# Kernel optimization log

Measured on AMD Instinct MI355X. Metric: run time of the kernel, lower is better.

The kernel has to match this reference:

```python
import jax, jax.numpy as jnp
import numpy as np
from jax import lax

NUM_LAYERS, C, HIDDEN = 3, 64, 128
B, H, W = 16, 128, 128
DC = C // 4  # partial-conv channels (dim_conv = dim // 4)


def _conv2d(x, w, b=None, groups=1):
    # x: [B,C,H,W], w: [O, C//groups, kh, kw], SAME padding, stride 1
    y = lax.conv_general_dilated(x, w, (1, 1), 'SAME',
                                 dimension_numbers=('NCHW', 'OIHW', 'NCHW'),
                                 feature_group_count=groups)
    return y if b is None else y + b[None, :, None, None]


def _pw(x, w, b):
    # 1x1x1 Conv3d at T=1 == pointwise channel mix. w: [O, C], b: [O]
    return jnp.einsum('oc,bchw->bohw', w, x) + b[None, :, None, None]


def _gelu(x):
    return jax.nn.gelu(x, approximate=False)  # torch nn.GELU default (erf)


def setup_inputs() -> dict:
    key = jax.random.key(0)
    ks = jax.random.split(key, 18)
    s = 0.1
    return {
        'x': jax.random.normal(ks[0], (B, C, H, W), jnp.float32),
        'wz1': jax.random.normal(ks[1], (NUM_LAYERS, C, C), jnp.float32) * s,
        'bz1': jax.random.normal(ks[2], (NUM_LAYERS, C), jnp.float32) * s,
        'wz2': jax.random.normal(ks[3], (NUM_LAYERS, C, C), jnp.float32) * s,
        'bz2': jax.random.normal(ks[4], (NUM_LAYERS, C), jnp.float32) * s,
        'wf1': jax.random.normal(ks[5], (NUM_LAYERS, C, C), jnp.float32) * s,
        'bf1': jax.random.normal(ks[6], (NUM_LAYERS, C), jnp.float32) * s,
        'wf2': jax.random.normal(ks[7], (NUM_LAYERS, C, C), jnp.float32) * s,
        'bf2': jax.random.normal(ks[8], (NUM_LAYERS, C), jnp.float32) * s,
        # FRFN
        'pconv_w': jax.random.normal(ks[9], (NUM_LAYERS, DC, DC, 3, 3), jnp.float32) * s,
        'lin1_w': jax.random.normal(ks[10], (NUM_LAYERS, C, 2 * HIDDEN), jnp.float32) * s,
        'lin1_b': jax.random.normal(ks[11], (NUM_LAYERS, 2 * HIDDEN), jnp.float32) * s,
        'dw_w': jax.random.normal(ks[12], (NUM_LAYERS, HIDDEN, 1, 3, 3), jnp.float32) * s,
        'dw_b': jax.random.normal(ks[13], (NUM_LAYERS, HIDDEN), jnp.float32) * s,
        'lin2_w': jax.random.normal(ks[14], (NUM_LAYERS, HIDDEN, C), jnp.float32) * s,
        'lin2_b': jax.random.normal(ks[15], (NUM_LAYERS, C), jnp.float32) * s,
        # conv_out: in_dim -> out_dim=1, 3x3
        'out_w': jax.random.normal(ks[16], (1, C, 3, 3), jnp.float32) * s,
        'out_b': jax.random.normal(ks[17], (1,), jnp.float32) * s,
    }


def reference(x, wz1, bz1, wz2, bz2, wf1, bf1, wf2, bf2,
              pconv_w, lin1_w, lin1_b, dw_w, dw_b, lin2_w, lin2_b,
              out_w, out_b):
    x_init = x
    for l in range(NUM_LAYERS):
        # ---- MHRB: time dim is 1 (x.unsqueeze(2)), so flips over dim 2 are
        # identities and the recurrence is a single step h = (1 - F) * Z.
        Z = jnp.tanh(_pw(jnp.tanh(_pw(x, wz1[l], bz1[l])), wz2[l], bz2[l]))
        F = jax.nn.sigmoid(_pw(jnp.tanh(_pw(x, wf1[l], bf1[l])), wf2[l], bf2[l]))
        x = (1.0 - F) * Z
        # ---- FRFN (operates on b (h w) c; equivalently on NCHW channel dim)
        res = x
        x1 = _conv2d(x[:, :DC], pconv_w[l])            # partial 3x3 conv, no bias
        x = jnp.concatenate([x1, x[:, DC:]], axis=1)
        h = _gelu(jnp.einsum('bchw,ck->bkhw', x, lin1_w[l])
                  + lin1_b[l][None, :, None, None])    # linear1 + GELU
        h1, h2 = h[:, :HIDDEN], h[:, HIDDEN:]          # chunk(2, dim=-1)
        h1 = _gelu(_conv2d(h1, dw_w[l], dw_b[l], groups=HIDDEN))  # dwconv + GELU
        g = h1 * h2                                    # gating
        x = (jnp.einsum('bkhw,kc->bchw', g, lin2_w[l])
             + lin2_b[l][None, :, None, None]) + res   # linear2 + residual
    return _conv2d(x + x_init, out_w, out_b)           # conv_out
```

## Files before the change

### kernel.cpp

```cpp
#include <hip/hip_runtime.h>
#include <hip/hip_bf16.h>

#define CC 64
#define HIDN 128
#define DCC 16
#define HH 128
#define WW 128
#define HWS (HH*WW)
#define BB 16
#define NPIX (BB*HWS)

typedef __hip_bfloat16 bf16;
typedef __attribute__((ext_vector_type(8))) unsigned short ushort8;
typedef __attribute__((ext_vector_type(4))) unsigned short ushort4v;
typedef __attribute__((ext_vector_type(4))) float float4v;
typedef __attribute__((ext_vector_type(8))) short bf16x8;
typedef __attribute__((ext_vector_type(4))) float f32x4;

__device__ __forceinline__ float rcp_fast(float x){ return __builtin_amdgcn_rcpf(x); }
__device__ __forceinline__ float ftanh(float x){
    float e = __expf(2.f*x);
    return 1.f - 2.f*rcp_fast(e + 1.f);
}
__device__ __forceinline__ float fsig(float x){
    return rcp_fast(1.f + __expf(-x));
}
__device__ __forceinline__ float fgelu(float x){
    return x * fsig(x*(1.5957691216f + 0.07135481283f*x*x));
}
__device__ __forceinline__ float b2f(bf16 v){ return __bfloat162float(v); }
__device__ __forceinline__ float u2f(unsigned short u){
    unsigned v = ((unsigned)u) << 16; return __uint_as_float(v);
}
__device__ __forceinline__ unsigned short f2u(float f){
    bf16 h = __float2bfloat16(f);
    return *reinterpret_cast<unsigned short*>(&h);
}
__device__ __forceinline__ bf16x8 packf(float4v a, float4v b){
    bf16x8 r;
    r[0]=(short)f2u(a.x); r[1]=(short)f2u(a.y); r[2]=(short)f2u(a.z); r[3]=(short)f2u(a.w);
    r[4]=(short)f2u(b.x); r[5]=(short)f2u(b.y); r[6]=(short)f2u(b.z); r[7]=(short)f2u(b.w);
    return r;
}

template<int F32>
__global__ __launch_bounds__(256,2) void k_gate(
    const float* __restrict__ xf, const bf16* __restrict__ xb,
    const float* __restrict__ wz1, const float* __restrict__ bz1,
    const float* __restrict__ wz2, const float* __restrict__ bz2,
    const float* __restrict__ wf1, const float* __restrict__ bf1,
    const float* __restrict__ wf2, const float* __restrict__ bf2,
    bf16* __restrict__ vout)
{
    __shared__ __align__(16) unsigned short xs[512*64];
    const int t = threadIdx.x;
    const int lane = t & 63;
    const int wv = t >> 6;
    const int col = lane & 15;
    const int g = lane >> 4;
    const int blk = blockIdx.x;
    const int b = blk >> 5;
    const int sp0 = (blk & 31) << 9;

    {
        const int ch = t & 63;
        const int wg = t >> 6;
        const size_t base = ((size_t)b*CC + ch)*HWS + sp0;
        #pragma unroll
        for (int i=0;i<16;++i){
            int bufpx = (wg*16 + i) << 3;
            ushort8 val;
            if (F32){
                float4v a = *reinterpret_cast<const float4v*>(xf + base + bufpx);
                float4v c = *reinterpret_cast<const float4v*>(xf + base + bufpx + 4);
                val[0]=f2u(a.x); val[1]=f2u(a.y); val[2]=f2u(a.z); val[3]=f2u(a.w);
                val[4]=f2u(c.x); val[5]=f2u(c.y); val[6]=f2u(c.z); val[7]=f2u(c.w);
            } else {
                val = *reinterpret_cast<const ushort8*>(xb + base + bufpx);
            }
            #pragma unroll
            for (int j=0;j<8;++j){
                int px = bufpx + j;
                *(unsigned short*)((char*)xs + px*128 + ((ch*2) ^ ((px&7)<<4))) = val[j];
            }
        }
    }

    bf16x8 Az1[4][2], Af1[4][2], Az2[4][2], Af2[4][2];
    #pragma unroll
    for (int ot=0; ot<4; ++ot){
        #pragma unroll
        for (int kh=0; kh<2; ++kh){
            const float* p;
            p = wz1 + (ot*16+col)*64 + kh*32 + g*8;
            Az1[ot][kh] = packf(*(const float4v*)p, *(const float4v*)(p+4));
            p = wf1 + (ot*16+col)*64 + kh*32 + g*8;
            Af1[ot][kh] = packf(*(const float4v*)p, *(const float4v*)(p+4));
            p = wz2 + (ot*16+col)*64 + kh*32 + g*4;
            Az2[ot][kh] = packf(*(const float4v*)p, *(const float4v*)(p+16));
            p = wf2 + (ot*16+col)*64 + kh*32 + g*4;
            Af2[ot][kh] = packf(*(const float4v*)p, *(const float4v*)(p+16));
        }
    }
    __syncthreads();

    bf16* vb = vout + (size_t)b*CC*HWS;

    for (int it = wv; it < 32; it += 4){
        const int lpx = it*16 + col;
        const int px = sp0 + lpx;
        bf16x8 Bx[2];
        Bx[0] = *(const bf16x8*)((char*)xs + lpx*128 + ((g*16) ^ ((lpx&7)<<4)));
        Bx[1] = *(const bf16x8*)((char*)xs + lpx*128 + ((64 + g*16) ^ ((lpx&7)<<4)));
        f32x4 Dz[4], Df[4];
        #pragma unroll
        for (int ot=0; ot<4; ++ot){
            Dz[ot] = *(const f32x4*)(bz1 + ot*16 + g*4);
            Df[ot] = *(const f32x4*)(bf1 + ot*16 + g*4);
        }
        #pragma unroll
        for (int kh=0; kh<2; ++kh)
            #pragma unroll
            for (int ot=0; ot<4; ++ot){
                Dz[ot] = __builtin_amdgcn_mfma_f32_16x16x32_bf16(Az1[ot][kh], Bx[kh], Dz[ot], 0,0,0);
                Df[ot] = __builtin_amdgcn_mfma_f32_16x16x32_bf16(Af1[ot][kh], Bx[kh], Df[ot], 0,0,0);
            }
        #pragma unroll
        for (int ot=0; ot<4; ++ot)
            #pragma unroll
            for (int r=0; r<4; ++r){
                Dz[ot][r] = ftanh(Dz[ot][r]);
                Df[ot][r] = ftanh(Df[ot][r]);
            }
        bf16x8 Bz[2], Bf[2];
        #pragma unroll
        for (int kh=0; kh<2; ++kh)
            #pragma unroll
            for (int j=0; j<4; ++j){
                Bz[kh][j]   = (short)f2u(Dz[2*kh][j]);
                Bz[kh][4+j] = (short)f2u(Dz[2*kh+1][j]);
                Bf[kh][j]   = (short)f2u(Df[2*kh][j]);
                Bf[kh][4+j] = (short)f2u(Df[2*kh+1][j]);
            }
        f32x4 Ez[4], Ef[4];
        #pragma unroll
        for (int ot=0; ot<4; ++ot){
            Ez[ot] = *(const f32x4*)(bz2 + ot*16 + g*4);
            Ef[ot] = *(const f32x4*)(bf2 + ot*16 + g*4);
        }
        #pragma unroll
        for (int kh=0; kh<2; ++kh)
            #pragma unroll
            for (int ot=0; ot<4; ++ot){
                Ez[ot] = __builtin_amdgcn_mfma_f32_16x16x32_bf16(Az2[ot][kh], Bz[kh], Ez[ot], 0,0,0);
                Ef[ot] = __builtin_amdgcn_mfma_f32_16x16x32_bf16(Af2[ot][kh], Bf[kh], Ef[ot], 0,0,0);
            }
        #pragma unroll
        for (int ot=0; ot<4; ++ot)
            #pragma unroll
            for (int r=0; r<4; ++r){
                float Zv = ftanh(Ez[ot][r]);
                float Fv = fsig(Ef[ot][r]);
                *reinterpret_cast<unsigned short*>(vb + (size_t)(ot*16+g*4+r)*HWS + px)
                    = f2u((1.f - Fv)*Zv);
            }
    }
}

__global__ __launch_bounds__(256) void k_pl1(
    const bf16* __restrict__ v, const float* __restrict__ pw,
    const float* __restrict__ l1w, const float* __restrict__ l1b,
    bf16* __restrict__ x1out, bf16* __restrict__ h1out)
{
    __shared__ __align__(16) unsigned short xs[256*64];
    __shared__ __align__(16) unsigned short vh[16][4][128];
    __shared__ __align__(16) unsigned short tr[4][32*66];
    const int t = threadIdx.x;
    const int lane = t & 63;
    const int wv = t >> 6;
    const int col = lane & 15;
    const int g = lane >> 4;
    const int blk = blockIdx.x;
    const int b = blk >> 6;
    const int y0 = (blk & 63) << 1;
    const int sp0 = y0 * WW;

    {
        const int ch = t & 63;
        const int wg = t >> 6;
        if (ch < DCC){
            int gy = y0 - 1 + wg;
            unsigned short* dst = &vh[ch][wg][0];
            if (gy >= 0 && gy < HH){
                const bf16* src = v + ((size_t)b*CC + ch)*HWS + (size_t)gy*WW;
                #pragma unroll
                for (int i=0;i<16;++i)
                    *reinterpret_cast<ushort8*>(dst + i*8) =
                        *reinterpret_cast<const ushort8*>(src + i*8);
            } else {
                #pragma unroll
                for (int i=0;i<16;++i){
                    ushort8 z;
                    #pragma unroll
                    for (int j=0;j<8;++j) z[j]=0;
                    *reinterpret_cast<ushort8*>(dst + i*8) = z;
                }
            }
        } else {
            const bf16* src = v + ((size_t)b*CC + ch)*HWS + sp0;
            #pragma unroll
            for (int i=0;i<8;++i){
                int bufpx = wg*64 + i*8;
                ushort8 val = *reinterpret_cast<const ushort8*>(src + bufpx);
                #pragma unroll
                for (int j=0;j<8;++j){
                    int px = bufpx + j;
                    *(unsigned short*)((char*)xs + px*128 + ((ch*2) ^ ((px&7)<<4))) = val[j];
                }
            }
        }
    }
    __syncthreads();

    {
        const int oc = t >> 4;
        const int px0 = (t & 15) << 3;
        float acc[2][8];
        #pragma unroll
        for (int r=0;r<2;++r)
            #pragma unroll
            for (int i=0;i<8;++i) acc[r][i]=0.f;
        #pragma unroll 1
        for (int ic=0; ic<DCC; ++ic){
            float m[4][10];
            #pragma unroll
            for (int row=0;row<4;++row){
                const unsigned short* rp = &vh[ic][row][px0];
                ushort8 mv = *reinterpret_cast<const ushort8*>(rp);
                #pragma unroll
                for (int i=0;i<8;++i) m[row][i+1] = u2f(mv[i]);
                m[row][0] = (px0>0)    ? u2f(rp[-1]) : 0.f;
                m[row][9] = (px0+8<WW) ? u2f(rp[8])  : 0.f;
            }
            const float* wp = pw + (size_t)(oc*DCC+ic)*9;
            #pragma unroll
            for (int ky=0;ky<3;++ky){
                float w0 = wp[ky*3+0], w1 = wp[ky*3+1], w2 = wp[ky*3+2];
                #pragma unroll
                for (int r=0;r<2;++r)
                    #pragma unroll
                    for (int i=0;i<8;++i)
                        acc[r][i] = fmaf(w0, m[r+ky][i],
                                    fmaf(w1, m[r+ky][i+1],
                                    fmaf(w2, m[r+ky][i+2], acc[r][i])));
            }
        }
        #pragma unroll
        for (int r=0;r<2;++r){
            ushort8 ov;
            #pragma unroll
            for (int i=0;i<8;++i){
                unsigned short uu = f2u(acc[r][i]);
                ov[i] = uu;
                int px = r*128 + px0 + i;
                *(unsigned short*)((char*)xs + px*128 + ((oc*2) ^ ((px&7)<<4))) = uu;
            }
            *reinterpret_cast<ushort8*>(x1out + ((size_t)b*DCC + oc)*HWS
                                        + (size_t)(y0+r)*WW + px0) = ov;
        }
    }
    __syncthreads();

    unsigned short* trw = &tr[wv][0];
    const int lpx0 = wv*64;

    #pragma unroll 1
    for (int oc=0; oc<4; ++oc){
        bf16x8 A1[2][2];
        #pragma unroll
        for (int t2=0;t2<2;++t2)
            #pragma unroll
            for (int kh=0;kh<2;++kh){
                bf16x8 fa;
                #pragma unroll
                for (int j=0;j<8;++j){
                    int cin = kh*32 + g*8 + j;
                    fa[j] = (short)f2u(l1w[cin*256 + oc*32 + t2*16 + col]);
                }
                A1[t2][kh]=fa;
            }
        #pragma unroll
        for (int lt=0;lt<4;++lt){
            int px = lpx0 + lt*16 + col;
            bf16x8 B0 = *(const bf16x8*)((char*)xs + px*128 + ((g*16) ^ ((px&7)<<4)));
            bf16x8 B1 = *(const bf16x8*)((char*)xs + px*128 + ((64 + g*16) ^ ((px&7)<<4)));
            f32x4 D0 = *(const f32x4*)(l1b + oc*32 + g*4);
            f32x4 D1 = *(const f32x4*)(l1b + oc*32 + 16 + g*4);
            D0 = __builtin_amdgcn_mfma_f32_16x16x32_bf16(A1[0][0], B0, D0, 0,0,0);
            D0 = __builtin_amdgcn_mfma_f32_16x16x32_bf16(A1[0][1], B1, D0, 0,0,0);
            D1 = __builtin_amdgcn_mfma_f32_16x16x32_bf16(A1[1][0], B0, D1, 0,0,0);
            D1 = __builtin_amdgcn_mfma_f32_16x16x32_bf16(A1[1][1], B1, D1, 0,0,0);
            int lp = lt*16 + col;
            #pragma unroll
            for (int rr=0;rr<4;++rr){
                trw[(g*4+rr)*66 + lp]    = f2u(fgelu(D0[rr]));
                trw[(16+g*4+rr)*66 + lp] = f2u(fgelu(D1[rr]));
            }
        }
        {
            int ch2 = lane >> 1;
            int half = lane & 1;
            const unsigned short* srcp = trw + ch2*66 + half*32;
            bf16* dst = h1out + ((size_t)(b*HIDN + oc*32 + ch2))*HWS + sp0 + lpx0 + half*32;
            #pragma unroll
            for (int i=0;i<4;++i){
                ushort8 u8 = *reinterpret_cast<const ushort8*>(srcp + i*8);
                *reinterpret_cast<ushort8*>(dst + i*8) = u8;
            }
        }
    }
}

__global__ __launch_bounds__(256) void k_wprep(
    const float* __restrict__ l1w_all, const float* __restrict__ w2_all,
    bf16* __restrict__ frag_all)
{
    const int l = blockIdx.x;
    const float* l1w = l1w_all + (size_t)l*CC*256;
    const float* w2  = w2_all  + (size_t)l*HIDN*CC;
    unsigned short* buf1 = (unsigned short*)(frag_all + (size_t)l*16384);
    unsigned short* buf2 = buf1 + 8192;
    const int t = threadIdx.x;
    const int lane = t & 63;
    const int col = lane & 15;
    const int g = lane >> 4;
    #pragma unroll
    for (int c4=0;c4<4;++c4){
        int combo = (t>>6)*4 + c4;
        {
            int cc = combo >> 2, t2 = (combo>>1)&1, kh = combo&1;
            #pragma unroll
            for (int j=0;j<8;++j){
                int cin = kh*32 + g*8 + j;
                buf1[(combo*64 + lane)*8 + j] =
                    f2u(l1w[cin*256 + 128 + cc*32 + t2*16 + col]);
            }
        }
        {
            int cc = combo >> 2, ot = combo & 3;
            #pragma unroll
            for (int j=0;j<8;++j){
                int k = cc*32 + ((j>>2)<<4) + (g<<2) + (j&3);
                buf2[(combo*64 + lane)*8 + j] = f2u(w2[k*64 + ot*16 + col]);
            }
        }
    }
}

__global__ __launch_bounds__(256) void k_dwA(
    const bf16* __restrict__ x1, const bf16* __restrict__ v,
    const bf16* __restrict__ h1, const bf16* __restrict__ wfrag,
    const float* __restrict__ l1b,
    const float* __restrict__ dww, const float* __restrict__ dwb,
    const float* __restrict__ l2b,
    bf16* __restrict__ xout,
    const float* __restrict__ xinit,
    bf16* __restrict__ xsum)
{
    __shared__ __align__(16) unsigned short xs[128*64];
    __shared__ __align__(16) unsigned short ubuf[2*8320];
    const int t = threadIdx.x;
    const int lane = t & 63;
    const int wv = t >> 6;
    const int col = lane & 15;
    const int g = lane >> 4;
    const int blk0 = blockIdx.x;
    const int blk = (blk0 & 7)*256 + (blk0 >> 3);
    const int b = blk >> 7;
    const int y = blk & 127;

    const int cj  = (t>>3) & 31;
    const int pxo = (t & 7) << 4;

    const unsigned short* buf1 = (const unsigned short*)wfrag;
    const unsigned short* buf2 = buf1 + 8192;

    ushort8 pfa[3], pfb[3];
    unsigned short pfl[3], pfr[3];
    float pw9[9], pbj;
    auto LOADCHUNK = [&](int cc){
        int chg = cc*32 + cj;
        const bf16* h1p = h1 + ((size_t)(b*HIDN + chg))*HWS;
        #pragma unroll
        for (int ky=0; ky<3; ++ky){
            int gy = y + ky - 1;
            if (gy >= 0 && gy < HH){
                const bf16* rp = h1p + (size_t)gy*WW + pxo;
                pfa[ky] = *reinterpret_cast<const ushort8*>(rp);
                pfb[ky] = *reinterpret_cast<const ushort8*>(rp+8);
                pfl[ky] = (pxo>0)     ? *reinterpret_cast<const unsigned short*>(rp-1)  : 0;
                pfr[ky] = (pxo+16<WW) ? *reinterpret_cast<const unsigned short*>(rp+16) : 0;
            } else {
                #pragma unroll
                for (int i=0;i<8;++i){ pfa[ky][i]=0; pfb[ky][i]=0; }
                pfl[ky]=0; pfr[ky]=0;
            }
        }
        #pragma unroll
        for (int i=0;i<9;++i) pw9[i] = dww[chg*9+i];
        pbj = dwb[chg];
    };

    LOADCHUNK(0);

    {
        const int ch = t & 63;
        const int wg = t >> 6;
        const bf16* src = (ch < DCC) ? x1 + ((size_t)b*DCC + ch)*HWS
                                     : v  + ((size_t)b*CC  + ch)*HWS;
        #pragma unroll
        for (int i=0;i<2;++i){
            int bufpx = (wg*2 + i) << 3;
            ushort8 val = *reinterpret_cast<const ushort8*>(src + (size_t)y*WW + bufpx);
            #pragma unroll
            for (int j=0;j<8;++j){
                int px = bufpx + j;
                *(unsigned short*)((char*)xs + px*128 + ((ch*2) ^ ((px&7)<<4))) = val[j];
            }
        }
    }
    __syncthreads();

    f32x4 Dx[2][4];
    #pragma unroll
    for (int q=0;q<2;++q)
        #pragma unroll
        for (int ot=0;ot<4;++ot)
            Dx[q][ot] = *(const f32x4*)(l2b + ot*16 + g*4);

    #pragma unroll 1
    for (int cc=0; cc<4; ++cc){
        unsigned short* ub = ubuf + (cc&1)*8320;
        ushort8 o0v, o1v;
        {
            float acc[16];
            #pragma unroll
            for (int i=0;i<16;++i) acc[i]=0.f;
            #pragma unroll
            for (int ky=0; ky<3; ++ky){
                float m[16];
                #pragma unroll
                for (int i=0;i<8;++i){ m[i]=u2f(pfa[ky][i]); m[8+i]=u2f(pfb[ky][i]); }
                float lf = u2f(pfl[ky]);
                float rt = u2f(pfr[ky]);
                float w0=pw9[ky*3], w1=pw9[ky*3+1], wv2=pw9[ky*3+2];
                #pragma unroll
                for (int i=0;i<16;++i){
                    float l  = i ? m[i-1] : lf;
                    float r_ = (i==15) ? rt : m[i+1];
                    acc[i] = fmaf(w0,l, fmaf(w1,m[i], fmaf(wv2,r_,acc[i])));
                }
            }
            #pragma unroll
            for (int i=0;i<8;++i){
                o0v[i] = f2u(fgelu(acc[i]+pbj));
                o1v[i] = f2u(fgelu(acc[8+i]+pbj));
            }
        }
        if (cc < 3) LOADCHUNK(cc+1);
        *(ushort8*)(ub + cj*260 + pxo)     = o0v;
        *(ushort8*)(ub + cj*260 + pxo + 8) = o1v;
        __syncthreads();
        {
            bf16x8 A1g[2][2];
            #pragma unroll
            for (int t2=0;t2<2;++t2)
                #pragma unroll
                for (int kh=0;kh<2;++kh){
                    int combo = (cc*2+t2)*2+kh;
                    ushort8 u = *reinterpret_cast<const ushort8*>(buf1 + (combo*64 + lane)*8);
                    bf16x8 f;
                    #pragma unroll
                    for (int j=0;j<8;++j) f[j]=(short)u[j];
                    A1g[t2][kh]=f;
                }
            bf16x8 A2[4];
            #pragma unroll
            for (int ot=0;ot<4;++ot){
                int combo = cc*4+ot;
                ushort8 u = *reinterpret_cast<const ushort8*>(buf2 + (combo*64 + lane)*8);
                bf16x8 f;
                #pragma unroll
                for (int j=0;j<8;++j) f[j]=(short)u[j];
                A2[ot] = f;
            }
            #pragma unroll
            for (int q=0;q<2;++q){
                int px = (wv*2+q)*16 + col;
                bf16x8 B0 = *(const bf16x8*)((char*)xs + px*128 + ((g*16) ^ ((px&7)<<4)));
                bf16x8 B1 = *(const bf16x8*)((char*)xs + px*128 + ((64 + g*16) ^ ((px&7)<<4)));
                f32x4 D0 = *(const f32x4*)(l1b + 128 + cc*32 + g*4);
                f32x4 D1 = *(const f32x4*)(l1b + 128 + cc*32 + 16 + g*4);
                D0 = __builtin_amdgcn_mfma_f32_16x16x32_bf16(A1g[0][0], B0, D0, 0,0,0);
                D0 = __builtin_amdgcn_mfma_f32_16x16x32_bf16(A1g[0][1], B1, D0, 0,0,0);
                D1 = __builtin_amdgcn_mfma_f32_16x16x32_bf16(A1g[1][0], B0, D1, 0,0,0);
                D1 = __builtin_amdgcn_mfma_f32_16x16x32_bf16(A1g[1][1], B1, D1, 0,0,0);
                bf16x8 Bg;
                #pragma unroll
                for (int j=0;j<4;++j){
                    float u0 = u2f(ub[(g*4+j)*260 + px]);
                    float u1 = u2f(ub[(16+g*4+j)*260 + px]);
                    Bg[j]   = (short)f2u(u0 * fgelu(D0[j]));
                    Bg[4+j] = (short)f2u(u1 * fgelu(D1[j]));
                }
                #pragma unroll
                for (int ot=0;ot<4;++ot)
                    Dx[q][ot] = __builtin_amdgcn_mfma_f32_16x16x32_bf16(A2[ot], Bg, Dx[q][ot], 0,0,0);
            }
        }
    }
    __syncthreads();
    #pragma unroll
    for (int q=0;q<2;++q)
        #pragma unroll
        for (int ot=0;ot<4;++ot)
            #pragma unroll
            for (int rr=0;rr<4;++rr)
                ubuf[(ot*16 + g*4 + rr)*136 + (wv*2+q)*16 + col] = f2u(Dx[q][ot][rr]);
    __syncthreads();
    {
        int ch  = t >> 2;
        int pxb = (t & 3) * 32;
        size_t off = ((size_t)(b*CC + ch))*HWS + (size_t)y*WW + pxb;
        #pragma unroll
        for (int i=0;i<4;++i){
            ushort8 dv = *reinterpret_cast<const ushort8*>(ubuf + ch*136 + pxb + i*8);
            ushort8 vv = *reinterpret_cast<const ushort8*>(v + off + i*8);
            ushort8 ov;
            float rv[8];
            #pragma unroll
            for (int j=0;j<8;++j){
                rv[j] = u2f(dv[j]) + u2f(vv[j]);
                ov[j] = f2u(rv[j]);
            }
            *reinterpret_cast<ushort8*>(xout + off + i*8) = ov;
            if (xinit){
                float4v x0 = *reinterpret_cast<const float4v*>(xinit + off + i*8);
                float4v x1v = *reinterpret_cast<const float4v*>(xinit + off + i*8 + 4);
                ushort8 sv;
                sv[0]=f2u(rv[0]+x0.x); sv[1]=f2u(rv[1]+x0.y);
                sv[2]=f2u(rv[2]+x0.z); sv[3]=f2u(rv[3]+x0.w);
                sv[4]=f2u(rv[4]+x1v.x); sv[5]=f2u(rv[5]+x1v.y);
                sv[6]=f2u(rv[6]+x1v.z); sv[7]=f2u(rv[7]+x1v.w);
                *reinterpret_cast<ushort8*>(xsum + off + i*8) = sv;
            }
        }
    }
}

__global__ __launch_bounds__(256) void k_final(
    const bf16* __restrict__ s, const float* __restrict__ w,
    const float* __restrict__ bias, float* __restrict__ out)
{
    int gid = blockIdx.x*256 + threadIdx.x;
    int b = gid >> 11;
    int sp8 = (gid & 2047) << 3;
    int y = sp8 >> 7, x0 = sp8 & 127;
    const bf16* sb = s + (size_t)b*CC*HWS;
    float acc[8];
    #pragma unroll
    for (int i=0;i<8;++i) acc[i] = bias[0];

    #pragma unroll 1
    for (int c=0;c<CC;++c){
        const bf16* ip = sb + (size_t)c*HWS;
        const float* wp = w + (size_t)c*9;
        #pragma unroll
        for (int ky=0;ky<3;++ky){
            int yy = y + ky - 1;
            float xv[10];
            if (yy >= 0 && yy < HH){
                const bf16* rp = ip + yy*WW + x0;
                ushort8 mv = *reinterpret_cast<const ushort8*>(rp);
                #pragma unroll
                for (int i=0;i<8;++i) xv[i+1]=u2f(mv[i]);
                xv[0] = (x0>0)    ? b2f(rp[-1]) : 0.f;
                xv[9] = (x0+8<WW) ? b2f(rp[8])  : 0.f;
            } else {
                #pragma unroll
                for (int i=0;i<10;++i) xv[i] = 0.f;
            }
            float w0 = wp[ky*3+0], w1 = wp[ky*3+1], w2 = wp[ky*3+2];
            #pragma unroll
            for (int i=0;i<8;++i)
                acc[i] = fmaf(w0, xv[i],
                         fmaf(w1, xv[i+1],
                         fmaf(w2, xv[i+2], acc[i])));
        }
    }
    float4v o0, o1;
    o0.x=acc[0]; o0.y=acc[1]; o0.z=acc[2]; o0.w=acc[3];
    o1.x=acc[4]; o1.y=acc[5]; o1.z=acc[6]; o1.w=acc[7];
    float* op = out + (size_t)gid*8;
    *reinterpret_cast<float4v*>(op)     = o0;
    *reinterpret_cast<float4v*>(op + 4) = o1;
}

extern "C" void kernel_launch(void* const* d_in, const int* in_sizes, int n_in,
                              void* d_out, int out_size, void* d_ws, size_t ws_size,
                              hipStream_t stream)
{
    const float* x    = (const float*)d_in[0];
    const float* wz1  = (const float*)d_in[1];
    const float* bz1  = (const float*)d_in[2];
    const float* wz2  = (const float*)d_in[3];
    const float* bz2  = (const float*)d_in[4];
    const float* wf1  = (const float*)d_in[5];
    const float* bf1  = (const float*)d_in[6];
    const float* wf2  = (const float*)d_in[7];
    const float* bf2  = (const float*)d_in[8];
    const float* pw   = (const float*)d_in[9];
    const float* l1w  = (const float*)d_in[10];
    const float* l1b  = (const float*)d_in[11];
    const float* dww  = (const float*)d_in[12];
    const float* dwb  = (const float*)d_in[13];
    const float* l2w  = (const float*)d_in[14];
    const float* l2b  = (const float*)d_in[15];
    const float* ow   = (const float*)d_in[16];
    const float* obb  = (const float*)d_in[17];

    char* ws = (char*)d_ws;
    bf16* xc    = (bf16*)(ws);
    bf16* v     = (bf16*)(ws + 33554432);
    bf16* x1    = (bf16*)(ws + 67108864);
    bf16* xsumb = (bf16*)(ws + 75497472);
    bf16* h1buf = (bf16*)(ws + 109051904);
    bf16* wfrag = (bf16*)(ws + 176160768);

    k_wprep<<<3, 256, 0, stream>>>(l1w, l2w, wfrag);
    for (int l=0;l<3;++l){
        if (l == 0)
            k_gate<1><<<512, 256, 0, stream>>>(x, nullptr,
                wz1 + l*CC*CC, bz1 + l*CC, wz2 + l*CC*CC, bz2 + l*CC,
                wf1 + l*CC*CC, bf1 + l*CC, wf2 + l*CC*CC, bf2 + l*CC, v);
        else
            k_gate<0><<<512, 256, 0, stream>>>(nullptr, xc,
                wz1 + l*CC*CC, bz1 + l*CC, wz2 + l*CC*CC, bz2 + l*CC,
                wf1 + l*CC*CC, bf1 + l*CC, wf2 + l*CC*CC, bf2 + l*CC, v);
        k_pl1  <<<NPIX/256, 256, 0, stream>>>(v, pw + l*DCC*DCC*9,
                l1w + l*CC*256, l1b + l*256, x1, h1buf);
        k_dwA  <<<BB*HH, 256, 0, stream>>>(x1, v, h1buf, wfrag + (size_t)l*16384,
                l1b + l*256,
                dww + l*HIDN*9, dwb + l*HIDN,
                l2b + l*CC,
                xc, (l==2) ? x : nullptr, xsumb);
    }
    k_final<<<NPIX/(256*8), 256, 0, stream>>>(xsumb, ow, obb, (float*)d_out);
}
```

Before: 673.0 us.

## Process two image rows per block in fused dwconv/gating/linear2 kernel

Each k_dwA block now handles two adjacent output rows instead of one, halving the grid. The depthwise 3x3 loads four input rows per channel chunk instead of three per output row, which reuses the shared halo rows. Weight fragment loads are also amortized over twice as many pixels. The double-buffered ub is replaced by one buffer plus an extra barrier per chunk. This costs more registers (Dx doubles, extra prefetch rows) and larger LDS, so occupancy may drop.

```diff
diff --git a/kernel.cpp b/kernel.cpp
--- a/kernel.cpp
+++ b/kernel.cpp
@@ -367,17 +367,17 @@
     const float* __restrict__ xinit,
     bf16* __restrict__ xsum)
 {
-    __shared__ __align__(16) unsigned short xs[128*64];
-    __shared__ __align__(16) unsigned short ubuf[2*8320];
+    __shared__ __align__(16) unsigned short xs[256*64];
+    __shared__ __align__(16) unsigned short ub[64*264];
     const int t = threadIdx.x;
     const int lane = t & 63;
     const int wv = t >> 6;
     const int col = lane & 15;
     const int g = lane >> 4;
     const int blk0 = blockIdx.x;
-    const int blk = (blk0 & 7)*256 + (blk0 >> 3);
-    const int b = blk >> 7;
-    const int y = blk & 127;
+    const int blk = (blk0 & 7)*128 + (blk0 >> 3);
+    const int b = blk >> 6;
+    const int y0 = (blk & 63) << 1;
 
     const int cj  = (t>>3) & 31;
     const int pxo = (t & 7) << 4;
@@ -385,15 +385,15 @@
     const unsigned short* buf1 = (const unsigned short*)wfrag;
     const unsigned short* buf2 = buf1 + 8192;
 
-    ushort8 pfa[3], pfb[3];
-    unsigned short pfl[3], pfr[3];
+    ushort8 pfa[4], pfb[4];
+    unsigned short pfl[4], pfr[4];
     float pw9[9], pbj;
     auto LOADCHUNK = [&](int cc){
         int chg = cc*32 + cj;
         const bf16* h1p = h1 + ((size_t)(b*HIDN + chg))*HWS;
         #pragma unroll
-        for (int ky=0; ky<3; ++ky){
-            int gy = y + ky - 1;
+        for (int ky=0; ky<4; ++ky){
+            int gy = y0 + ky - 1;
             if (gy >= 0 && gy < HH){
                 const bf16* rp = h1p + (size_t)gy*WW + pxo;
                 pfa[ky] = *reinterpret_cast<const ushort8*>(rp);
@@ -418,10 +418,11 @@
         const int wg = t >> 6;
         const bf16* src = (ch < DCC) ? x1 + ((size_t)b*DCC + ch)*HWS
                                      : v  + ((size_t)b*CC  + ch)*HWS;
-        #pragma unroll
-        for (int i=0;i<2;++i){
-            int bufpx = (wg*2 + i) << 3;
-            ushort8 val = *reinterpret_cast<const ushort8*>(src + (size_t)y*WW + bufpx);
+        const size_t base = (size_t)y0*WW;
+        #pragma unroll
+        for (int i=0;i<8;++i){
+            int bufpx = wg*64 + i*8;
+            ushort8 val = *reinterpret_cast<const ushort8*>(src + base + bufpx);
             #pragma unroll
             for (int j=0;j<8;++j){
                 int px = bufpx + j;
@@ -431,18 +432,17 @@
     }
     __syncthreads();
 
-    f32x4 Dx[2][4];
+    f32x4 Dx[4][4];
     #pragma unroll
-    for (int q=0;q<2;++q)
+    for (int q=0;q<4;++q)
         #pragma unroll
         for (int ot=0;ot<4;++ot)
             Dx[q][ot] = *(const f32x4*)(l2b + ot*16 + g*4);
 
     #pragma unroll 1
     for (int cc=0; cc<4; ++cc){
-        unsigned short* ub = ubuf + (cc&1)*8320;
-        ushort8 o0v, o1v;
-        {
+        #pragma unroll
+        for (int r=0;r<2;++r){
             float acc[16];
             #pragma unroll
             for (int i=0;i<16;++i) acc[i]=0.f;
@@ -450,9 +450,9 @@
             for (int ky=0; ky<3; ++ky){
                 float m[16];
                 #pragma unroll
-                for (int i=0;i<8;++i){ m[i]=u2f(pfa[ky][i]); m[8+i]=u2f(pfb[ky][i]); }
-                float lf = u2f(pfl[ky]);
-                float rt = u2f(pfr[ky]);
+                for (int i=0;i<8;++i){ m[i]=u2f(pfa[r+ky][i]); m[8+i]=u2f(pfb[r+ky][i]); }
+                float lf = u2f(pfl[r+ky]);
+                float rt = u2f(pfr[r+ky]);
                 float w0=pw9[ky*3], w1=pw9[ky*3+1], wv2=pw9[ky*3+2];
                 #pragma unroll
                 for (int i=0;i<16;++i){
@@ -461,15 +461,16 @@
                     acc[i] = fmaf(w0,l, fmaf(w1,m[i], fmaf(wv2,r_,acc[i])));
                 }
             }
+            ushort8 o0v, o1v;
             #pragma unroll
             for (int i=0;i<8;++i){
                 o0v[i] = f2u(fgelu(acc[i]+pbj));
                 o1v[i] = f2u(fgelu(acc[8+i]+pbj));
             }
+            *(ushort8*)(ub + cj*528 + r*264 + pxo)     = o0v;
+            *(ushort8*)(ub + cj*528 + r*264 + pxo + 8) = o1v;
         }
         if (cc < 3) LOADCHUNK(cc+1);
-        *(ushort8*)(ub + cj*260 + pxo)     = o0v;
-        *(ushort8*)(ub + cj*260 + pxo + 8) = o1v;
         __syncthreads();
         {
             bf16x8 A1g[2][2];
@@ -495,10 +496,11 @@
                 A2[ot] = f;
             }
             #pragma unroll
-            for (int q=0;q<2;++q){
-                int px = (wv*2+q)*16 + col;
-                bf16x8 B0 = *(const bf16x8*)((char*)xs + px*128 + ((g*16) ^ ((px&7)<<4)));
-                bf16x8 B1 = *(const bf16x8*)((char*)xs + px*128 + ((64 + g*16) ^ ((px&7)<<4)));
+            for (int q=0;q<4;++q){
+                int pxs = (wv*4+q)*16 + col;
+                int row = pxs >> 7, px = pxs & 127;
+                bf16x8 B0 = *(const bf16x8*)((char*)xs + pxs*128 + ((g*16) ^ ((pxs&7)<<4)));
+                bf16x8 B1 = *(const bf16x8*)((char*)xs + pxs*128 + ((64 + g*16) ^ ((pxs&7)<<4)));
                 f32x4 D0 = *(const f32x4*)(l1b + 128 + cc*32 + g*4);
                 f32x4 D1 = *(const f32x4*)(l1b + 128 + cc*32 + 16 + g*4);
                 D0 = __builtin_amdgcn_mfma_f32_16x16x32_bf16(A1g[0][0], B0, D0, 0,0,0);
@@ -508,8 +510,8 @@
                 bf16x8 Bg;
                 #pragma unroll
                 for (int j=0;j<4;++j){
-                    float u0 = u2f(ub[(g*4+j)*260 + px]);
-                    float u1 = u2f(ub[(16+g*4+j)*260 + px]);
+                    float u0 = u2f(ub[(g*4+j)*528 + row*264 + px]);
+                    float u1 = u2f(ub[(16+g*4+j)*528 + row*264 + px]);
                     Bg[j]   = (short)f2u(u0 * fgelu(D0[j]));
                     Bg[4+j] = (short)f2u(u1 * fgelu(D1[j]));
                 }
@@ -518,23 +520,24 @@
                     Dx[q][ot] = __builtin_amdgcn_mfma_f32_16x16x32_bf16(A2[ot], Bg, Dx[q][ot], 0,0,0);
             }
         }
-    }
-    __syncthreads();
+        __syncthreads();
+    }
     #pragma unroll
-    for (int q=0;q<2;++q)
+    for (int q=0;q<4;++q)
         #pragma unroll
         for (int ot=0;ot<4;++ot)
             #pragma unroll
             for (int rr=0;rr<4;++rr)
-                ubuf[(ot*16 + g*4 + rr)*136 + (wv*2+q)*16 + col] = f2u(Dx[q][ot][rr]);
+                ub[(ot*16 + g*4 + rr)*264 + (wv*4+q)*16 + col] = f2u(Dx[q][ot][rr]);
     __syncthreads();
     {
-        int ch  = t >> 2;
-        int pxb = (t & 3) * 32;
-        size_t off = ((size_t)(b*CC + ch))*HWS + (size_t)y*WW + pxb;
-        #pragma unroll
-        for (int i=0;i<4;++i){
-            ushort8 dv = *reinterpret_cast<const ushort8*>(ubuf + ch*136 + pxb + i*8);
+        int ch   = t >> 2;
+        int part = t & 3;
+        int pxb  = part*64;
+        size_t off = ((size_t)(b*CC + ch))*HWS + (size_t)y0*WW + pxb;
+        #pragma unroll
+        for (int i=0;i<8;++i){
+            ushort8 dv = *reinterpret_cast<const ushort8*>(ub + ch*264 + pxb + i*8);
             ushort8 vv = *reinterpret_cast<const ushort8*>(v + off + i*8);
             ushort8 ov;
             float rv[8];
@@ -649,7 +652,7 @@
                 wf1 + l*CC*CC, bf1 + l*CC, wf2 + l*CC*CC, bf2 + l*CC, v);
         k_pl1  <<<NPIX/256, 256, 0, stream>>>(v, pw + l*DCC*DCC*9,
                 l1w + l*CC*256, l1b + l*256, x1, h1buf);
-        k_dwA  <<<BB*HH, 256, 0, stream>>>(x1, v, h1buf, wfrag + (size_t)l*16384,
+        k_dwA  <<<BB*HH/2, 256, 0, stream>>>(x1, v, h1buf, wfrag + (size_t)l*16384,
                 l1b + l*256,
                 dww + l*HIDN*9, dwb + l*HIDN,
                 l2b + l*CC,
```

Result: no change. 672.9 us (-0.0%).

## Process two image rows per block in fused dwconv/MLP kernel with 512 threads

Applied to the files above, without the earlier changes.

The fused dwconv+gating+linear2 kernel now handles two consecutive rows per block using 512 threads, halving the grid. Each thread maps to one of two rows for the depthwise conv stage, and the MFMA stage covers 256 pixels. The double-buffered u buffer becomes a per-row buffer with an extra barrier at the end of each chunk iteration. This amortizes per-block weight fragment loads and setup over more pixels, but adds a sync per chunk, drops the double buffering, and raises LDS use per block, which may cut occupancy.

```diff
diff --git a/kernel.cpp b/kernel.cpp
--- a/kernel.cpp
+++ b/kernel.cpp
@@ -357,7 +357,7 @@
     }
 }
 
-__global__ __launch_bounds__(256) void k_dwA(
+__global__ __launch_bounds__(512) void k_dwA(
     const bf16* __restrict__ x1, const bf16* __restrict__ v,
     const bf16* __restrict__ h1, const bf16* __restrict__ wfrag,
     const float* __restrict__ l1b,
@@ -367,20 +367,22 @@
     const float* __restrict__ xinit,
     bf16* __restrict__ xsum)
 {
-    __shared__ __align__(16) unsigned short xs[128*64];
-    __shared__ __align__(16) unsigned short ubuf[2*8320];
+    __shared__ __align__(16) unsigned short xs[256*64];
+    __shared__ __align__(16) unsigned short ub[16896];
     const int t = threadIdx.x;
     const int lane = t & 63;
     const int wv = t >> 6;
     const int col = lane & 15;
     const int g = lane >> 4;
     const int blk0 = blockIdx.x;
-    const int blk = (blk0 & 7)*256 + (blk0 >> 3);
-    const int b = blk >> 7;
-    const int y = blk & 127;
-
-    const int cj  = (t>>3) & 31;
-    const int pxo = (t & 7) << 4;
+    const int blk = (blk0 & 7)*128 + (blk0 >> 3);
+    const int b = blk >> 6;
+    const int y0 = (blk & 63) << 1;
+
+    const int grp = t & 15;
+    const int drow = grp >> 3;
+    const int pxo  = (grp & 7) << 4;
+    const int cj   = t >> 4;
 
     const unsigned short* buf1 = (const unsigned short*)wfrag;
     const unsigned short* buf2 = buf1 + 8192;
@@ -393,7 +395,7 @@
         const bf16* h1p = h1 + ((size_t)(b*HIDN + chg))*HWS;
         #pragma unroll
         for (int ky=0; ky<3; ++ky){
-            int gy = y + ky - 1;
+            int gy = y0 + drow + ky - 1;
             if (gy >= 0 && gy < HH){
                 const bf16* rp = h1p + (size_t)gy*WW + pxo;
                 pfa[ky] = *reinterpret_cast<const ushort8*>(rp);
@@ -418,10 +420,11 @@
         const int wg = t >> 6;
         const bf16* src = (ch < DCC) ? x1 + ((size_t)b*DCC + ch)*HWS
                                      : v  + ((size_t)b*CC  + ch)*HWS;
-        #pragma unroll
-        for (int i=0;i<2;++i){
-            int bufpx = (wg*2 + i) << 3;
-            ushort8 val = *reinterpret_cast<const ushort8*>(src + (size_t)y*WW + bufpx);
+        const size_t base = (size_t)y0*WW;
+        #pragma unroll
+        for (int i=0;i<4;++i){
+            int bufpx = wg*32 + i*8;
+            ushort8 val = *reinterpret_cast<const ushort8*>(src + base + bufpx);
             #pragma unroll
             for (int j=0;j<8;++j){
                 int px = bufpx + j;
@@ -440,7 +443,6 @@
 
     #pragma unroll 1
     for (int cc=0; cc<4; ++cc){
-        unsigned short* ub = ubuf + (cc&1)*8320;
         ushort8 o0v, o1v;
         {
             float acc[16];
@@ -468,8 +470,8 @@
             }
         }
         if (cc < 3) LOADCHUNK(cc+1);
-        *(ushort8*)(ub + cj*260 + pxo)     = o0v;
-        *(ushort8*)(ub + cj*260 + pxo + 8) = o1v;
+        *(ushort8*)(ub + drow*8320 + cj*260 + pxo)     = o0v;
+        *(ushort8*)(ub + drow*8320 + cj*260 + pxo + 8) = o1v;
         __syncthreads();
         {
             bf16x8 A1g[2][2];
@@ -496,9 +498,10 @@
             }
             #pragma unroll
             for (int q=0;q<2;++q){
-                int px = (wv*2+q)*16 + col;
-                bf16x8 B0 = *(const bf16x8*)((char*)xs + px*128 + ((g*16) ^ ((px&7)<<4)));
-                bf16x8 B1 = *(const bf16x8*)((char*)xs + px*128 + ((64 + g*16) ^ ((px&7)<<4)));
+                int pxs = (wv*2+q)*16 + col;
+                int row = pxs >> 7, px = pxs & 127;
+                bf16x8 B0 = *(const bf16x8*)((char*)xs + pxs*128 + ((g*16) ^ ((pxs&7)<<4)));
+                bf16x8 B1 = *(const bf16x8*)((char*)xs + pxs*128 + ((64 + g*16) ^ ((pxs&7)<<4)));
                 f32x4 D0 = *(const f32x4*)(l1b + 128 + cc*32 + g*4);
                 f32x4 D1 = *(const f32x4*)(l1b + 128 + cc*32 + 16 + g*4);
                 D0 = __builtin_amdgcn_mfma_f32_16x16x32_bf16(A1g[0][0], B0, D0, 0,0,0);
@@ -508,8 +511,8 @@
                 bf16x8 Bg;
                 #pragma unroll
                 for (int j=0;j<4;++j){
-                    float u0 = u2f(ub[(g*4+j)*260 + px]);
-                    float u1 = u2f(ub[(16+g*4+j)*260 + px]);
+                    float u0 = u2f(ub[row*8320 + (g*4+j)*260 + px]);
+                    float u1 = u2f(ub[row*8320 + (16+g*4+j)*260 + px]);
                     Bg[j]   = (short)f2u(u0 * fgelu(D0[j]));
                     Bg[4+j] = (short)f2u(u1 * fgelu(D1[j]));
                 }
@@ -518,23 +521,24 @@
                     Dx[q][ot] = __builtin_amdgcn_mfma_f32_16x16x32_bf16(A2[ot], Bg, Dx[q][ot], 0,0,0);
             }
         }
-    }
-    __syncthreads();
+        __syncthreads();
+    }
     #pragma unroll
     for (int q=0;q<2;++q)
         #pragma unroll
         for (int ot=0;ot<4;++ot)
             #pragma unroll
             for (int rr=0;rr<4;++rr)
-                ubuf[(ot*16 + g*4 + rr)*136 + (wv*2+q)*16 + col] = f2u(Dx[q][ot][rr]);
+                ub[(ot*16 + g*4 + rr)*264 + (wv*2+q)*16 + col] = f2u(Dx[q][ot][rr]);
     __syncthreads();
     {
-        int ch  = t >> 2;
-        int pxb = (t & 3) * 32;
-        size_t off = ((size_t)(b*CC + ch))*HWS + (size_t)y*WW + pxb;
+        int ch   = t >> 3;
+        int part = t & 7;
+        int pxb  = part*32;
+        size_t off = ((size_t)(b*CC + ch))*HWS + (size_t)y0*WW + pxb;
         #pragma unroll
         for (int i=0;i<4;++i){
-            ushort8 dv = *reinterpret_cast<const ushort8*>(ubuf + ch*136 + pxb + i*8);
+            ushort8 dv = *reinterpret_cast<const ushort8*>(ub + ch*264 + pxb + i*8);
             ushort8 vv = *reinterpret_cast<const ushort8*>(v + off + i*8);
             ushort8 ov;
             float rv[8];
@@ -649,7 +653,7 @@
                 wf1 + l*CC*CC, bf1 + l*CC, wf2 + l*CC*CC, bf2 + l*CC, v);
         k_pl1  <<<NPIX/256, 256, 0, stream>>>(v, pw + l*DCC*DCC*9,
                 l1w + l*CC*256, l1b + l*256, x1, h1buf);
-        k_dwA  <<<BB*HH, 256, 0, stream>>>(x1, v, h1buf, wfrag + (size_t)l*16384,
+        k_dwA  <<<BB*HH/2, 512, 0, stream>>>(x1, v, h1buf, wfrag + (size_t)l*16384,
                 l1b + l*256,
                 dww + l*HIDN*9, dwb + l*HIDN,
                 l2b + l*CC,
```

After: 742.2 us. 10.3% more time.
